# Kernel tuning notes

Hardware: AMD Instinct MI355X
Metric: run time of the kernel (lower is better)

The kernel has to match this reference:

```python
import jax, jax.numpy as jnp
import numpy as np
import math

D_MODEL = 512
N_HEADS = 8
D_FF = 2048
FACTOR = 5


def _layernorm(x, g, b, eps=1e-5):
    mu = jnp.mean(x, axis=-1, keepdims=True)
    var = jnp.mean((x - mu) ** 2, axis=-1, keepdims=True)
    return (x - mu) / jnp.sqrt(var + eps) * g + b


def setup_inputs() -> dict:
    key = jax.random.key(0)
    ks = jax.random.split(key, 12)
    B, L, D, F = 4, 2048, D_MODEL, D_FF
    sample_k = FACTOR * int(math.ceil(math.log(L)))  # 40
    x = jax.random.normal(ks[0], (B, L, D), dtype=jnp.float32)
    index_sample = jax.random.randint(ks[1], (L, sample_k), 0, L)
    s = 0.02
    inp = {
        'x': x,
        'index_sample': index_sample,
        'Wq': jax.random.normal(ks[2], (D, D), jnp.float32) * s, 'bq': jnp.zeros((D,), jnp.float32),
        'Wk': jax.random.normal(ks[3], (D, D), jnp.float32) * s, 'bk': jnp.zeros((D,), jnp.float32),
        'Wv': jax.random.normal(ks[4], (D, D), jnp.float32) * s, 'bv': jnp.zeros((D,), jnp.float32),
        'Wo': jax.random.normal(ks[5], (D, D), jnp.float32) * s, 'bo': jnp.zeros((D,), jnp.float32),
        'W1': jax.random.normal(ks[6], (F, D), jnp.float32) * s, 'b1': jnp.zeros((F,), jnp.float32),
        'W2': jax.random.normal(ks[7], (D, F), jnp.float32) * s, 'b2': jnp.zeros((D,), jnp.float32),
        'g1': jnp.ones((D,), jnp.float32), 'be1': jnp.zeros((D,), jnp.float32),
        'g2': jnp.ones((D,), jnp.float32), 'be2': jnp.zeros((D,), jnp.float32),
    }
    return inp


def _encoder_layer(x, index_sample, Wq, bq, Wk, bk, Wv, bv, Wo, bo, W1, b1, W2, b2, g1, be1, g2, be2):
    B, L, D = x.shape
    H = N_HEADS
    dk = D // H
    n_top = FACTOR * int(math.ceil(math.log(L)))  # 40; sparse branch since L*L > 40*40

    def split_heads(t):  # (B,L,D) -> (B,H,L,dk)
        return t.reshape(B, L, H, dk).transpose(0, 2, 1, 3)

    q = split_heads(x @ Wq.T + bq)
    k = split_heads(x @ Wk.T + bk)
    v = split_heads(x @ Wv.T + bv)

    # --- ProbSparse sampling: K_sample[b,h,i,j] = k[b,h,index_sample[i,j]] ---
    k_sample = k[:, :, index_sample, :]                      # (B,H,L,sample_k,dk)
    scores_sample = jnp.einsum('bhid,bhijd->bhij', q, k_sample)
    M = jnp.max(scores_sample, axis=-1) - jnp.sum(scores_sample, axis=-1) / L  # (B,H,L)
    _, top_idx = jax.lax.top_k(M, n_top)                     # (B,H,n_top)

    q_red = jnp.take_along_axis(q, top_idx[..., None], axis=2)  # (B,H,n_top,dk)
    scores_red = jnp.einsum('bhnd,bhkd->bhnk', q_red, k)        # NOTE: unscaled, as in source sparse branch

    bi = jnp.arange(B)[:, None, None]
    hi = jnp.arange(H)[None, :, None]
    scores = jnp.zeros((B, H, L, L), x.dtype).at[bi, hi, top_idx].set(scores_red)

    attn = jax.nn.softmax(scores, axis=-1)  # all-zero rows -> uniform (mean of V)
    ctx = jnp.einsum('bhqk,bhkd->bhqd', attn, v).transpose(0, 2, 1, 3).reshape(B, L, D)
    attn_out = ctx @ Wo.T + bo

    h1 = _layernorm(x + attn_out, g1, be1)
    ff = jax.nn.gelu(h1 @ W1.T + b1, approximate=False) @ W2.T + b2
    return _layernorm(h1 + ff, g2, be2)


def reference(x, index_sample, Wq, bq, Wk, bk, Wv, bv, Wo, bo, W1, b1, W2, b2, g1, be1, g2, be2):
    return _encoder_layer(x, index_sample, Wq, bq, Wk, bk, Wv, bv, Wo, bo,
                          W1, b1, W2, b2, g1, be1, g2, be2)
```

## Files before the change

kernel.cpp:

```cpp
#include <hip/hip_runtime.h>
#include <math.h>

#define L_SEQ   2048
#define DMODEL  512
#define NHEADS  8
#define DK      64
#define DFF     2048
#define BATCH   4
#define NTOP    40
#define MROWS   (BATCH*L_SEQ)
#define NCH     8
#define CHSZ    256
#define QPAD    48

typedef _Float16 f16;
typedef __attribute__((ext_vector_type(8))) _Float16 f16x8;
typedef __attribute__((ext_vector_type(8))) short    s16x8;
typedef __attribute__((ext_vector_type(4))) float    f32x4;

__device__ __forceinline__ ushort f2h_bits(float x) {
    f16 h = (f16)x;
    return __builtin_bit_cast(ushort, h);
}
__device__ __forceinline__ float h2f(ushort u) {
    return (float)__builtin_bit_cast(f16, u);
}

#define GLL16(gp, lp) \
    __builtin_amdgcn_global_load_lds((const __attribute__((address_space(1))) void*)(gp), \
                                     (__attribute__((address_space(3))) void*)(lp), 16, 0, 0)

template<int SPLIT3, int ACT, int OUTMODE>
__global__ __launch_bounds__(256)
void gemm16(const ushort* __restrict__ Ah, const ushort* __restrict__ Al,
            const ushort* __restrict__ Wh, const ushort* __restrict__ Wl,
            const float* __restrict__ bias,
            float* __restrict__ Cf, ushort* __restrict__ C16,
            int M, int N, int K)
{
    __shared__ __align__(16) ushort sAh[128*32];
    __shared__ __align__(16) ushort sBh[128*32];
    __shared__ __align__(16) ushort sAl[SPLIT3 ? 128*32 : 8];
    __shared__ __align__(16) ushort sBl[SPLIT3 ? 128*32 : 8];

    const int tid  = threadIdx.x;
    const int m0   = blockIdx.y * 128, n0 = blockIdx.x * 128;
    const int wid  = tid >> 6, lane = tid & 63;
    const int wr   = (wid >> 1) * 64;
    const int wc   = (wid & 1) * 64;
    const int lr   = lane & 15;
    const int ko   = (lane >> 4) * 8;

    f32x4 acc[4][4];
#pragma unroll
    for (int i = 0; i < 4; ++i)
#pragma unroll
        for (int j = 0; j < 4; ++j) acc[i][j] = (f32x4){0.f, 0.f, 0.f, 0.f};

    const int sr = tid >> 2, sc = (tid & 3) * 8;
    const size_t gA = (size_t)(m0 + sr) * K + sc;
    const size_t gB = (size_t)(n0 + sr) * K + sc;
    const int l0 = tid * 8, l1 = tid * 8 + 2048;

    for (int k0 = 0; k0 < K; k0 += 32) {
        GLL16(Ah + gA + k0,                sAh + l0);
        GLL16(Ah + gA + (size_t)64*K + k0, sAh + l1);
        GLL16(Wh + gB + k0,                sBh + l0);
        GLL16(Wh + gB + (size_t)64*K + k0, sBh + l1);
        if (SPLIT3) {
            GLL16(Al + gA + k0,                sAl + l0);
            GLL16(Al + gA + (size_t)64*K + k0, sAl + l1);
            GLL16(Wl + gB + k0,                sBl + l0);
            GLL16(Wl + gB + (size_t)64*K + k0, sBl + l1);
        }
        __syncthreads();

        f16x8 ah[4], bh[4], al[4], bl[4];
#pragma unroll
        for (int i = 0; i < 4; ++i) {
            ah[i] = *(const f16x8*)&sAh[(wr + i*16 + lr) * 32 + ko];
            bh[i] = *(const f16x8*)&sBh[(wc + i*16 + lr) * 32 + ko];
            if (SPLIT3) {
                al[i] = *(const f16x8*)&sAl[(wr + i*16 + lr) * 32 + ko];
                bl[i] = *(const f16x8*)&sBl[(wc + i*16 + lr) * 32 + ko];
            }
        }
#pragma unroll
        for (int i = 0; i < 4; ++i)
#pragma unroll
            for (int j = 0; j < 4; ++j) {
                acc[i][j] = __builtin_amdgcn_mfma_f32_16x16x32_f16(ah[i], bh[j], acc[i][j], 0, 0, 0);
                if (SPLIT3) {
                    acc[i][j] = __builtin_amdgcn_mfma_f32_16x16x32_f16(ah[i], bl[j], acc[i][j], 0, 0, 0);
                    acc[i][j] = __builtin_amdgcn_mfma_f32_16x16x32_f16(al[i], bh[j], acc[i][j], 0, 0, 0);
                }
            }
        __syncthreads();
    }

    const int r0 = m0 + wr + (lane >> 4) * 4;
#pragma unroll
    for (int i = 0; i < 4; ++i)
#pragma unroll
        for (int j = 0; j < 4; ++j) {
            const int col = n0 + wc + j * 16 + lr;
            const float bb = bias[col];
#pragma unroll
            for (int qq = 0; qq < 4; ++qq) {
                const int row = r0 + i * 16 + qq;
                float vv = acc[i][j][qq] + bb;
                if (ACT == 1) vv = 0.5f * vv * (1.f + erff(vv * 0.70710678118654752f));
                if (OUTMODE == 0 || OUTMODE == 2) Cf[(size_t)row * N + col] = vv;
                if (OUTMODE == 1 || OUTMODE == 2) C16[(size_t)row * N + col] = f2h_bits(vv);
                if (OUTMODE == 3)
                    C16[((size_t)(row >> 11) * 512 + (col >> 6) * 64 + (col & 63)) * 2048 + (row & 2047)] = f2h_bits(vv);
            }
        }
}

__device__ __forceinline__ void split8(const float* __restrict__ s,
                                       ushort* __restrict__ hi, ushort* __restrict__ lo)
{
    s16x8 h8, l8;
#pragma unroll
    for (int j = 0; j < 8; ++j) {
        float x = s[j];
        f16 hh = (f16)x;
        float r = x - (float)hh;
        f16 ll = (f16)r;
        h8[j] = (short)__builtin_bit_cast(ushort, hh);
        l8[j] = (short)__builtin_bit_cast(ushort, ll);
    }
    *(s16x8*)hi = h8;
    *(s16x8*)lo = l8;
}
__device__ __forceinline__ void cvt8(const float* __restrict__ s, ushort* __restrict__ d)
{
    s16x8 h8;
#pragma unroll
    for (int j = 0; j < 8; ++j) h8[j] = (short)f2h_bits(s[j]);
    *(s16x8*)d = h8;
}

__global__ __launch_bounds__(256)
void split_x(const float* __restrict__ x, ushort* __restrict__ xh, ushort* __restrict__ xl)
{
    const int t = blockIdx.x * 256 + threadIdx.x;
    split8(x + (size_t)t * 8, xh + (size_t)t * 8, xl + (size_t)t * 8);
}

__global__ __launch_bounds__(256)
void conv_weights(const float* __restrict__ Wq, const float* __restrict__ Wk,
                  const float* __restrict__ Wv, const float* __restrict__ Wo,
                  const float* __restrict__ W1, const float* __restrict__ W2,
                  ushort* wqh, ushort* wql, ushort* wkh, ushort* wkl,
                  ushort* wvh, ushort* woh, ushort* w1h, ushort* w2h)
{
    const int t = blockIdx.x * 256 + threadIdx.x;
    const int e = t * 8;
    const int S = DMODEL * DMODEL;
    if      (e < S)           split8(Wq + e,           wqh + e,           wql + e);
    else if (e < 2*S)         split8(Wk + (e -   S),   wkh + (e -   S),   wkl + (e -   S));
    else if (e < 3*S)         cvt8  (Wv + (e - 2*S),   wvh + (e - 2*S));
    else if (e < 4*S)         cvt8  (Wo + (e - 3*S),   woh + (e - 3*S));
    else if (e < 4*S + DFF*DMODEL) cvt8(W1 + (e - 4*S), w1h + (e - 4*S));
    else                      cvt8  (W2 + (e - 4*S - DFF*DMODEL), w2h + (e - 4*S - DFF*DMODEL));
}

__global__ __launch_bounds__(256, 4)
void sample_scores(const float* __restrict__ q, const float* __restrict__ k,
                   const int* __restrict__ idxs, float* __restrict__ Mout)
{
    __shared__ float4 qs[4][128];

    const int bid = blockIdx.x;
    const int xcd = bid & 7;
    const int b   = xcd >> 1;
    const int chunk = (bid >> 3) * 2 + (xcd & 1);
    const int wid = threadIdx.x >> 6, lane = threadIdx.x & 63;
    const int i = chunk * 4 + wid;
    const int jsub = lane >> 3, c = lane & 7;

    {
        const float4* qrow = (const float4*)&q[((size_t)(b * L_SEQ + i)) * DMODEL];
        qs[wid][lane]      = qrow[lane];
        qs[wid][lane + 64] = qrow[lane + 64];
    }
    __syncthreads();

    const float4* kb = (const float4*)&k[(size_t)b * L_SEQ * DMODEL];

    float mx = -1e30f, sm = 0.f;
#pragma unroll
    for (int jb = 0; jb < 5; ++jb) {
        const int kidx = idxs[i * NTOP + jb * 8 + jsub];
        const float4* krow = kb + (size_t)kidx * (DMODEL / 4);
        float hacc[8];
#pragma unroll
        for (int u = 0; u < 8; ++u) hacc[u] = 0.f;
#pragma unroll
        for (int t = 0; t < 16; ++t) {
            const int p = t * 8 + c;
            const float4 kv = krow[p];
            const float4 qv = qs[wid][p];
            float d = 0.f;
            d = fmaf(qv.x, kv.x, d);
            d = fmaf(qv.y, kv.y, d);
            d = fmaf(qv.z, kv.z, d);
            d = fmaf(qv.w, kv.w, d);
            hacc[t >> 1] += d;
        }
#pragma unroll
        for (int s = 1; s < 8; s <<= 1)
#pragma unroll
            for (int u = 0; u < 8; ++u) hacc[u] += __shfl_xor(hacc[u], s);
        float sel = hacc[0];
#pragma unroll
        for (int u = 1; u < 8; ++u) sel = (c == u) ? hacc[u] : sel;
        mx = fmaxf(mx, sel);
        sm += sel;
    }
#pragma unroll
    for (int s = 8; s < 64; s <<= 1) {
        mx = fmaxf(mx, __shfl_xor(mx, s));
        sm += __shfl_xor(sm, s);
    }
    if (jsub == 0)
        Mout[((size_t)(b * NHEADS + c)) * L_SEQ + i] = mx - sm * (1.0f / (float)L_SEQ);
}

__global__ __launch_bounds__(256)
void topk40(const float* __restrict__ Mstat, int* __restrict__ top_idx)
{
    const int bh = blockIdx.x;
    __shared__ float vals[L_SEQ];
    __shared__ float wv[4];
    __shared__ int   wi[4];
    const int tid = threadIdx.x;
    const int lane = tid & 63, wid = tid >> 6;
    for (int t = tid; t < L_SEQ; t += 256) vals[t] = Mstat[(size_t)bh * L_SEQ + t];
    __syncthreads();

    for (int n = 0; n < NTOP; ++n) {
        float bv = -1e30f; int bi = L_SEQ;
#pragma unroll
        for (int r = 0; r < 8; ++r) {
            const int t = tid + r * 256;
            float vvv = vals[t];
            if (vvv > bv) { bv = vvv; bi = t; }
        }
#pragma unroll
        for (int s = 32; s > 0; s >>= 1) {
            float ov = __shfl_xor(bv, s); int oi = __shfl_xor(bi, s);
            if (ov > bv || (ov == bv && oi < bi)) { bv = ov; bi = oi; }
        }
        if (lane == 0) { wv[wid] = bv; wi[wid] = bi; }
        __syncthreads();
        if (tid == 0) {
            float fb = wv[0]; int fi = wi[0];
#pragma unroll
            for (int w = 1; w < 4; ++w)
                if (wv[w] > fb || (wv[w] == fb && wi[w] < fi)) { fb = wv[w]; fi = wi[w]; }
            top_idx[bh * NTOP + n] = fi;
            vals[fi] = -1e30f;
        }
        __syncthreads();
    }
}

__global__ __launch_bounds__(256)
void vmean_kernel(const ushort* __restrict__ vt, float* __restrict__ vmean)
{
    const int bh = blockIdx.x;
    const int wid = threadIdx.x >> 6, lane = threadIdx.x & 63;
#pragma unroll
    for (int dd = 0; dd < 16; ++dd) {
        const int d = wid * 16 + dd;
        const ushort* row = vt + ((size_t)bh * 64 + d) * 2048;
        float s = 0.f;
#pragma unroll
        for (int it = 0; it < 4; ++it) {
            s16x8 vv = *(const s16x8*)&row[it * 512 + lane * 8];
#pragma unroll
            for (int j = 0; j < 8; ++j) s += h2f((ushort)vv[j]);
        }
#pragma unroll
        for (int st = 1; st < 64; st <<= 1) s += __shfl_xor(s, st);
        if (lane == 0) vmean[bh * DK + d] = s * (1.0f / (float)L_SEQ);
    }
}

__global__ __launch_bounds__(256)
void fill_ctx(const float* __restrict__ vmean, ushort* __restrict__ ctx)
{
    const int t = blockIdx.x * 256 + threadIdx.x;
    const int e = t * 8;
    const int col = e & (DMODEL - 1);
    const int row = e >> 9;
    const int b = row >> 11;
    const int h = col >> 6, d = col & 63;
    const float* vm = &vmean[(b * 8 + h) * DK + d];
    s16x8 o;
#pragma unroll
    for (int j = 0; j < 8; ++j) o[j] = (short)f2h_bits(vm[j]);
    *(s16x8*)&ctx[e] = o;
}

__global__ __launch_bounds__(256, 1)
void attn_flash(const float* __restrict__ q, const ushort* __restrict__ k16,
                const ushort* __restrict__ vt16, const int* __restrict__ top_idx,
                float* __restrict__ part_o, float* __restrict__ part_ml)
{
    __shared__ __align__(16) ushort K_lds [CHSZ * 64];
    __shared__ __align__(16) ushort Vt_lds[64 * CHSZ];
    __shared__ __align__(16) ushort Q_lds [QPAD * 64];
    __shared__ __align__(16) ushort P_lds [QPAD * CHSZ];
    __shared__ float red_max[4][QPAD];
    __shared__ float red_sum[4][QPAD];

    const int bh = blockIdx.x >> 3, ch = blockIdx.x & 7;
    const int b = bh >> 3, h = bh & 7;
    const int tid = threadIdx.x;
    const int wid = tid >> 6, lane = tid & 63;
    const int lr = lane & 15, ks = lane >> 4;

    {
        const ushort* kbase = k16 + ((size_t)b * L_SEQ + ch * CHSZ) * DMODEL + h * DK;
#pragma unroll
        for (int it = 0; it < 8; ++it) {
            const int qi2 = wid * 8 + it;
            const int row = qi2 * 8 + (lane >> 3);
            const int g = (lane & 7) ^ (row & 7);
            GLL16(kbase + (size_t)row * DMODEL + g * 8, K_lds + qi2 * 512 + lane * 8);
        }
        const ushort* vtb = vt16 + ((size_t)bh * 64) * 2048 + ch * CHSZ;
#pragma unroll
        for (int it = 0; it < 8; ++it) {
            const int qi2 = wid * 8 + it;
            const int drow = qi2 * 2 + (lane >> 5);
            const int g = (lane & 31) ^ (drow & 7);
            GLL16(vtb + (size_t)drow * 2048 + g * 8, Vt_lds + qi2 * 512 + lane * 8);
        }
    }
    if (tid < QPAD * 4) {
        const int r = tid >> 2, part = tid & 3;
        s16x8 w0, w1;
        if (r < NTOP) {
            const int qi = top_idx[bh * NTOP + r];
            const float* qp = q + ((size_t)b * L_SEQ + qi) * DMODEL + h * DK + part * 16;
#pragma unroll
            for (int u = 0; u < 8; ++u) { w0[u] = (short)f2h_bits(qp[u]); w1[u] = (short)f2h_bits(qp[u + 8]); }
        } else {
#pragma unroll
            for (int u = 0; u < 8; ++u) { w0[u] = 0; w1[u] = 0; }
        }
        const int g0 = part * 2;
        *(s16x8*)((char*)Q_lds + r * 128 + (((g0    ) ^ (r & 7)) << 4)) = w0;
        *(s16x8*)((char*)Q_lds + r * 128 + (((g0 + 1) ^ (r & 7)) << 4)) = w1;
    }
    __syncthreads();

    f16x8 af[3][2], bf[4][2];
#pragma unroll
    for (int i = 0; i < 3; ++i)
#pragma unroll
        for (int kt = 0; kt < 2; ++kt) {
            const int row = i * 16 + lr;
            const int g = (kt * 4 + ks) ^ (row & 7);
            af[i][kt] = *(const f16x8*)((const char*)Q_lds + row * 128 + g * 16);
        }
#pragma unroll
    for (int j = 0; j < 4; ++j)
#pragma unroll
        for (int kt = 0; kt < 2; ++kt) {
            const int row = wid * 64 + j * 16 + lr;
            const int g = (kt * 4 + ks) ^ (row & 7);
            bf[j][kt] = *(const f16x8*)((const char*)K_lds + row * 128 + g * 16);
        }
    f32x4 acc[3][4];
#pragma unroll
    for (int i = 0; i < 3; ++i)
#pragma unroll
        for (int j = 0; j < 4; ++j) acc[i][j] = (f32x4){0.f, 0.f, 0.f, 0.f};
#pragma unroll
    for (int i = 0; i < 3; ++i)
#pragma unroll
        for (int j = 0; j < 4; ++j)
#pragma unroll
            for (int kt = 0; kt < 2; ++kt)
                acc[i][j] = __builtin_amdgcn_mfma_f32_16x16x32_f16(af[i][kt], bf[j][kt], acc[i][j], 0, 0, 0);

    float mrow[3][4];
#pragma unroll
    for (int i = 0; i < 3; ++i)
#pragma unroll
        for (int r = 0; r < 4; ++r) {
            float m = acc[i][0][r];
            m = fmaxf(m, acc[i][1][r]); m = fmaxf(m, acc[i][2][r]); m = fmaxf(m, acc[i][3][r]);
            mrow[i][r] = m;
        }
#pragma unroll
    for (int s = 1; s < 16; s <<= 1)
#pragma unroll
        for (int i = 0; i < 3; ++i)
#pragma unroll
            for (int r = 0; r < 4; ++r) mrow[i][r] = fmaxf(mrow[i][r], __shfl_xor(mrow[i][r], s));
    if (lr == 0)
#pragma unroll
        for (int i = 0; i < 3; ++i)
#pragma unroll
            for (int r = 0; r < 4; ++r) red_max[wid][i * 16 + ks * 4 + r] = mrow[i][r];
    __syncthreads();
    float mc[3][4];
#pragma unroll
    for (int i = 0; i < 3; ++i)
#pragma unroll
        for (int r = 0; r < 4; ++r) {
            const int row = i * 16 + ks * 4 + r;
            mc[i][r] = fmaxf(fmaxf(red_max[0][row], red_max[1][row]),
                             fmaxf(red_max[2][row], red_max[3][row]));
        }

    float srow[3][4];
#pragma unroll
    for (int i = 0; i < 3; ++i)
#pragma unroll
        for (int r = 0; r < 4; ++r) srow[i][r] = 0.f;
#pragma unroll
    for (int i = 0; i < 3; ++i)
#pragma unroll
        for (int j = 0; j < 4; ++j)
#pragma unroll
            for (int r = 0; r < 4; ++r) {
                const float p = expf(acc[i][j][r] - mc[i][r]);
                srow[i][r] += p;
                const int row = i * 16 + ks * 4 + r;
                const int cc = wid * 64 + j * 16 + lr;
                const int g = (cc >> 3) ^ (row & 7);
                *(ushort*)((char*)P_lds + row * 512 + g * 16 + (cc & 7) * 2) = f2h_bits(p);
            }
#pragma unroll
    for (int s = 1; s < 16; s <<= 1)
#pragma unroll
        for (int i = 0; i < 3; ++i)
#pragma unroll
            for (int r = 0; r < 4; ++r) srow[i][r] += __shfl_xor(srow[i][r], s);
    if (lr == 0)
#pragma unroll
        for (int i = 0; i < 3; ++i)
#pragma unroll
            for (int r = 0; r < 4; ++r) red_sum[wid][i * 16 + ks * 4 + r] = srow[i][r];
    __syncthreads();

    if (wid == 0 && lr == 0) {
#pragma unroll
        for (int i = 0; i < 3; ++i)
#pragma unroll
            for (int r = 0; r < 4; ++r) {
                const int row = i * 16 + ks * 4 + r;
                const float lc = red_sum[0][row] + red_sum[1][row] + red_sum[2][row] + red_sum[3][row];
                part_ml[(((size_t)bh * NCH + ch) * QPAD + row) * 2 + 0] = mc[i][r];
                part_ml[(((size_t)bh * NCH + ch) * QPAD + row) * 2 + 1] = lc;
            }
    }

    f32x4 acc2[3];
#pragma unroll
    for (int i = 0; i < 3; ++i) acc2[i] = (f32x4){0.f, 0.f, 0.f, 0.f};
#pragma unroll
    for (int kt = 0; kt < 8; ++kt) {
        f16x8 vb;
        {
            const int row = wid * 16 + lr;
            const int g = (kt * 4 + ks) ^ (row & 7);
            vb = *(const f16x8*)((const char*)Vt_lds + row * 512 + g * 16);
        }
#pragma unroll
        for (int i = 0; i < 3; ++i) {
            const int row = i * 16 + lr;
            const int g = (kt * 4 + ks) ^ (row & 7);
            const f16x8 pa = *(const f16x8*)((const char*)P_lds + row * 512 + g * 16);
            acc2[i] = __builtin_amdgcn_mfma_f32_16x16x32_f16(pa, vb, acc2[i], 0, 0, 0);
        }
    }
#pragma unroll
    for (int i = 0; i < 3; ++i)
#pragma unroll
        for (int r = 0; r < 4; ++r) {
            const int row = i * 16 + ks * 4 + r;
            const int d = wid * 16 + lr;
            part_o[((((size_t)bh * NCH + ch) * QPAD) + row) * 64 + d] = acc2[i][r];
        }
}

__global__ __launch_bounds__(256)
void attn_combine(const float* __restrict__ part_o, const float* __restrict__ part_ml,
                  const int* __restrict__ top_idx, ushort* __restrict__ ctx)
{
    const int bh = blockIdx.x;
    const int b = bh >> 3, h = bh & 7;
    const int d = threadIdx.x & 63, qg = threadIdx.x >> 6;
#pragma unroll
    for (int u = 0; u < 10; ++u) {
        const int qq = qg * 10 + u;
        float mv[NCH], lv[NCH];
        float m = -1e30f;
#pragma unroll
        for (int c = 0; c < NCH; ++c) {
            mv[c] = part_ml[(((size_t)bh * NCH + c) * QPAD + qq) * 2 + 0];
            lv[c] = part_ml[(((size_t)bh * NCH + c) * QPAD + qq) * 2 + 1];
            m = fmaxf(m, mv[c]);
        }
        float l = 0.f, o = 0.f;
#pragma unroll
        for (int c = 0; c < NCH; ++c) {
            const float e = expf(mv[c] - m);
            l += e * lv[c];
            o += e * part_o[((((size_t)bh * NCH + c) * QPAD) + qq) * 64 + d];
        }
        const int qi = top_idx[bh * NTOP + qq];
        ctx[((size_t)b * L_SEQ + qi) * DMODEL + h * DK + d] = f2h_bits(o / l);
    }
}

template<int W16>
__global__ __launch_bounds__(256)
void ln_residual(const float* __restrict__ a, const float* __restrict__ bsrc,
                 const float* __restrict__ g, const float* __restrict__ be,
                 float* __restrict__ out, ushort* __restrict__ out16)
{
    const int row = blockIdx.x; const int tid = threadIdx.x;
    const size_t base = (size_t)row * DMODEL;
    float x0 = a[base + tid]       + bsrc[base + tid];
    float x1 = a[base + 256 + tid] + bsrc[base + 256 + tid];

    __shared__ float red[256];
    red[tid] = x0 + x1; __syncthreads();
    for (int st = 128; st > 0; st >>= 1) { if (tid < st) red[tid] += red[tid + st]; __syncthreads(); }
    const float mu = red[0] * (1.0f / (float)DMODEL);
    __syncthreads();

    const float d0 = x0 - mu, d1 = x1 - mu;
    red[tid] = d0 * d0 + d1 * d1; __syncthreads();
    for (int st = 128; st > 0; st >>= 1) { if (tid < st) red[tid] += red[tid + st]; __syncthreads(); }
    const float var = red[0] * (1.0f / (float)DMODEL);
    const float rstd = 1.0f / sqrtf(var + 1e-5f);

    const float y0 = d0 * rstd * g[tid]       + be[tid];
    const float y1 = d1 * rstd * g[256 + tid] + be[256 + tid];
    out[base + tid]       = y0;
    out[base + 256 + tid] = y1;
    if (W16) {
        out16[base + tid]       = f2h_bits(y0);
        out16[base + 256 + tid] = f2h_bits(y1);
    }
}

extern "C" void kernel_launch(void* const* d_in, const int* in_sizes, int n_in,
                              void* d_out, int out_size, void* d_ws, size_t ws_size,
                              hipStream_t stream)
{
    const float* x    = (const float*)d_in[0];
    const int*   idxs = (const int*)  d_in[1];
    const float* Wq = (const float*)d_in[2];  const float* bq = (const float*)d_in[3];
    const float* Wk = (const float*)d_in[4];  const float* bk = (const float*)d_in[5];
    const float* Wv = (const float*)d_in[6];  const float* bv = (const float*)d_in[7];
    const float* Wo = (const float*)d_in[8];  const float* bo = (const float*)d_in[9];
    const float* W1 = (const float*)d_in[10]; const float* b1 = (const float*)d_in[11];
    const float* W2 = (const float*)d_in[12]; const float* b2 = (const float*)d_in[13];
    const float* g1 = (const float*)d_in[14]; const float* be1= (const float*)d_in[15];
    const float* g2 = (const float*)d_in[16]; const float* be2= (const float*)d_in[17];

    const size_t MD = (size_t)MROWS * DMODEL;
    char* W = (char*)d_ws;
    ushort* xh   = (ushort*)(W);
    ushort* xl   = (ushort*)(W + 2*MD);
    float*  q    = (float*) (W + 4*MD);
    float*  k    = (float*) (W + 8*MD);
    ushort* k16  = (ushort*)(W + 12*MD);
    ushort* vt16 = (ushort*)(W + 14*MD);
    ushort* ctx16= (ushort*)(W + 16*MD);
    float*  att  = (float*) (W);
    float*  h1   = (float*) (W + 4*MD);
    ushort* h116 = (ushort*)(W + 8*MD);
    ushort* mid16= (ushort*)(W + 10*MD);
    ushort* wqh  = (ushort*)(W + 18*MD);
    ushort* wql  = wqh + DMODEL*DMODEL;
    ushort* wkh  = wql + DMODEL*DMODEL;
    ushort* wkl  = wkh + DMODEL*DMODEL;
    ushort* wvh  = wkl + DMODEL*DMODEL;
    ushort* woh  = wvh + DMODEL*DMODEL;
    ushort* w1h  = woh + DMODEL*DMODEL;
    ushort* w2h  = w1h + DFF*DMODEL;
    float*  Mstat = (float*)(w2h + DMODEL*DFF);
    float*  vmean = Mstat + (size_t)BATCH * NHEADS * L_SEQ;
    int*    top_idx = (int*)(vmean + BATCH * NHEADS * DK);
    float*  part_o  = (float*)(top_idx + BATCH * NHEADS * NTOP);
    float*  part_ml = part_o + (size_t)BATCH * NHEADS * NCH * QPAD * 64;

    dim3 blk(256);

    split_x<<<dim3(MD / 2048), blk, 0, stream>>>(x, xh, xl);
    conv_weights<<<dim3(1536), blk, 0, stream>>>(Wq, Wk, Wv, Wo, W1, W2,
                                                 wqh, wql, wkh, wkl, wvh, woh, w1h, w2h);

    gemm16<1,0,0><<<dim3(DMODEL/128, MROWS/128), blk, 0, stream>>>(xh, xl, wqh, wql, bq, q,   nullptr, MROWS, DMODEL, DMODEL);
    gemm16<1,0,2><<<dim3(DMODEL/128, MROWS/128), blk, 0, stream>>>(xh, xl, wkh, wkl, bk, k,   k16,     MROWS, DMODEL, DMODEL);
    gemm16<0,0,3><<<dim3(DMODEL/128, MROWS/128), blk, 0, stream>>>(xh, nullptr, wvh, nullptr, bv, nullptr, vt16, MROWS, DMODEL, DMODEL);

    sample_scores<<<dim3(2048), blk, 0, stream>>>(q, k, idxs, Mstat);
    topk40<<<dim3(BATCH*NHEADS), blk, 0, stream>>>(Mstat, top_idx);
    vmean_kernel<<<dim3(BATCH*NHEADS), blk, 0, stream>>>(vt16, vmean);
    fill_ctx<<<dim3(MD/2048), blk, 0, stream>>>(vmean, ctx16);
    attn_flash<<<dim3(BATCH*NHEADS*NCH), blk, 0, stream>>>(q, k16, vt16, top_idx, part_o, part_ml);
    attn_combine<<<dim3(BATCH*NHEADS), blk, 0, stream>>>(part_o, part_ml, top_idx, ctx16);

    gemm16<0,0,0><<<dim3(DMODEL/128, MROWS/128), blk, 0, stream>>>(ctx16, nullptr, woh, nullptr, bo, att, nullptr, MROWS, DMODEL, DMODEL);
    ln_residual<1><<<dim3(MROWS), blk, 0, stream>>>(x, att, g1, be1, h1, h116);

    gemm16<0,1,1><<<dim3(DFF/128, MROWS/128), blk, 0, stream>>>(h116, nullptr, w1h, nullptr, b1, nullptr, mid16, MROWS, DFF, DMODEL);
    gemm16<0,0,0><<<dim3(DMODEL/128, MROWS/128), blk, 0, stream>>>(mid16, nullptr, w2h, nullptr, b2, att, nullptr, MROWS, DMODEL, DFF);
    ln_residual<0><<<dim3(MROWS), blk, 0, stream>>>(h1, att, g2, be2, (float*)d_out, nullptr);
}
```

Baseline: 334.5 us.

## Batch QKV GEMMs into one launch, split-K the N=512 GEMMs, merge prep kernels

Merges the three Q/K/V projection GEMMs into one grid-z launch and folds the x-split and weight-conversion kernels into a single prep launch. The Wo and W2 GEMMs (N=512, 256 blocks) become split-K over two halves, writing two fp32 partials that the LayerNorm kernels sum together with the bias. The aim is to double block count on these small-grid GEMMs for better CU fill on a 256-CU part and to cut launch overhead. The cost is extra fp32 partial traffic and a larger workspace layout.

New measurement: 286.2 us. -14.5%, faster.

```diff
diff --git a/kernel.cpp b/kernel.cpp
--- a/kernel.cpp
+++ b/kernel.cpp
@@ -30,18 +30,27 @@
     __builtin_amdgcn_global_load_lds((const __attribute__((address_space(1))) void*)(gp), \
                                      (__attribute__((address_space(3))) void*)(lp), 16, 0, 0)
 
-template<int SPLIT3, int ACT, int OUTMODE>
-__global__ __launch_bounds__(256)
-void gemm16(const ushort* __restrict__ Ah, const ushort* __restrict__ Al,
-            const ushort* __restrict__ Wh, const ushort* __restrict__ Wl,
-            const float* __restrict__ bias,
-            float* __restrict__ Cf, ushort* __restrict__ C16,
-            int M, int N, int K)
+__global__ __launch_bounds__(256)
+void gemm_qkv(const ushort* __restrict__ xh, const ushort* __restrict__ xl,
+              const ushort* __restrict__ wqh, const ushort* __restrict__ wql,
+              const ushort* __restrict__ wkh, const ushort* __restrict__ wkl,
+              const ushort* __restrict__ wvh,
+              const float* __restrict__ bq, const float* __restrict__ bk,
+              const float* __restrict__ bv,
+              float* __restrict__ qo, float* __restrict__ kf,
+              ushort* __restrict__ k16, ushort* __restrict__ vt16)
 {
     __shared__ __align__(16) ushort sAh[128*32];
     __shared__ __align__(16) ushort sBh[128*32];
-    __shared__ __align__(16) ushort sAl[SPLIT3 ? 128*32 : 8];
-    __shared__ __align__(16) ushort sBl[SPLIT3 ? 128*32 : 8];
+    __shared__ __align__(16) ushort sAl[128*32];
+    __shared__ __align__(16) ushort sBl[128*32];
+
+    const int z = blockIdx.z;
+    const bool s3 = (z < 2);
+    const ushort* Wh = (z == 0) ? wqh : (z == 1) ? wkh : wvh;
+    const ushort* Wl = (z == 0) ? wql : wkl;
+    const float*  bias = (z == 0) ? bq : (z == 1) ? bk : bv;
+    const int K = DMODEL, N = DMODEL;
 
     const int tid  = threadIdx.x;
     const int m0   = blockIdx.y * 128, n0 = blockIdx.x * 128;
@@ -63,13 +72,13 @@
     const int l0 = tid * 8, l1 = tid * 8 + 2048;
 
     for (int k0 = 0; k0 < K; k0 += 32) {
-        GLL16(Ah + gA + k0,                sAh + l0);
-        GLL16(Ah + gA + (size_t)64*K + k0, sAh + l1);
+        GLL16(xh + gA + k0,                sAh + l0);
+        GLL16(xh + gA + (size_t)64*K + k0, sAh + l1);
         GLL16(Wh + gB + k0,                sBh + l0);
         GLL16(Wh + gB + (size_t)64*K + k0, sBh + l1);
-        if (SPLIT3) {
-            GLL16(Al + gA + k0,                sAl + l0);
-            GLL16(Al + gA + (size_t)64*K + k0, sAl + l1);
+        if (s3) {
+            GLL16(xl + gA + k0,                sAl + l0);
+            GLL16(xl + gA + (size_t)64*K + k0, sAl + l1);
             GLL16(Wl + gB + k0,                sBl + l0);
             GLL16(Wl + gB + (size_t)64*K + k0, sBl + l1);
         }
@@ -80,7 +89,7 @@
         for (int i = 0; i < 4; ++i) {
             ah[i] = *(const f16x8*)&sAh[(wr + i*16 + lr) * 32 + ko];
             bh[i] = *(const f16x8*)&sBh[(wc + i*16 + lr) * 32 + ko];
-            if (SPLIT3) {
+            if (s3) {
                 al[i] = *(const f16x8*)&sAl[(wr + i*16 + lr) * 32 + ko];
                 bl[i] = *(const f16x8*)&sBl[(wc + i*16 + lr) * 32 + ko];
             }
@@ -90,7 +99,7 @@
 #pragma unroll
             for (int j = 0; j < 4; ++j) {
                 acc[i][j] = __builtin_amdgcn_mfma_f32_16x16x32_f16(ah[i], bh[j], acc[i][j], 0, 0, 0);
-                if (SPLIT3) {
+                if (s3) {
                     acc[i][j] = __builtin_amdgcn_mfma_f32_16x16x32_f16(ah[i], bl[j], acc[i][j], 0, 0, 0);
                     acc[i][j] = __builtin_amdgcn_mfma_f32_16x16x32_f16(al[i], bh[j], acc[i][j], 0, 0, 0);
                 }
@@ -108,12 +117,147 @@
 #pragma unroll
             for (int qq = 0; qq < 4; ++qq) {
                 const int row = r0 + i * 16 + qq;
+                const float vv = acc[i][j][qq] + bb;
+                if (z == 0) {
+                    qo[(size_t)row * N + col] = vv;
+                } else if (z == 1) {
+                    kf [(size_t)row * N + col] = vv;
+                    k16[(size_t)row * N + col] = f2h_bits(vv);
+                } else {
+                    vt16[((size_t)(row >> 11) * 512 + (col >> 6) * 64 + (col & 63)) * 2048 + (row & 2047)] = f2h_bits(vv);
+                }
+            }
+        }
+}
+
+template<int ACT>
+__global__ __launch_bounds__(256)
+void gemm16(const ushort* __restrict__ Ah, const ushort* __restrict__ Wh,
+            const float* __restrict__ bias, ushort* __restrict__ C16,
+            int M, int N, int K)
+{
+    __shared__ __align__(16) ushort sAh[128*32];
+    __shared__ __align__(16) ushort sBh[128*32];
+
+    const int tid  = threadIdx.x;
+    const int m0   = blockIdx.y * 128, n0 = blockIdx.x * 128;
+    const int wid  = tid >> 6, lane = tid & 63;
+    const int wr   = (wid >> 1) * 64;
+    const int wc   = (wid & 1) * 64;
+    const int lr   = lane & 15;
+    const int ko   = (lane >> 4) * 8;
+
+    f32x4 acc[4][4];
+#pragma unroll
+    for (int i = 0; i < 4; ++i)
+#pragma unroll
+        for (int j = 0; j < 4; ++j) acc[i][j] = (f32x4){0.f, 0.f, 0.f, 0.f};
+
+    const int sr = tid >> 2, sc = (tid & 3) * 8;
+    const size_t gA = (size_t)(m0 + sr) * K + sc;
+    const size_t gB = (size_t)(n0 + sr) * K + sc;
+    const int l0 = tid * 8, l1 = tid * 8 + 2048;
+
+    for (int k0 = 0; k0 < K; k0 += 32) {
+        GLL16(Ah + gA + k0,                sAh + l0);
+        GLL16(Ah + gA + (size_t)64*K + k0, sAh + l1);
+        GLL16(Wh + gB + k0,                sBh + l0);
+        GLL16(Wh + gB + (size_t)64*K + k0, sBh + l1);
+        __syncthreads();
+
+        f16x8 ah[4], bh[4];
+#pragma unroll
+        for (int i = 0; i < 4; ++i) {
+            ah[i] = *(const f16x8*)&sAh[(wr + i*16 + lr) * 32 + ko];
+            bh[i] = *(const f16x8*)&sBh[(wc + i*16 + lr) * 32 + ko];
+        }
+#pragma unroll
+        for (int i = 0; i < 4; ++i)
+#pragma unroll
+            for (int j = 0; j < 4; ++j)
+                acc[i][j] = __builtin_amdgcn_mfma_f32_16x16x32_f16(ah[i], bh[j], acc[i][j], 0, 0, 0);
+        __syncthreads();
+    }
+
+    const int r0 = m0 + wr + (lane >> 4) * 4;
+#pragma unroll
+    for (int i = 0; i < 4; ++i)
+#pragma unroll
+        for (int j = 0; j < 4; ++j) {
+            const int col = n0 + wc + j * 16 + lr;
+            const float bb = bias[col];
+#pragma unroll
+            for (int qq = 0; qq < 4; ++qq) {
+                const int row = r0 + i * 16 + qq;
                 float vv = acc[i][j][qq] + bb;
                 if (ACT == 1) vv = 0.5f * vv * (1.f + erff(vv * 0.70710678118654752f));
-                if (OUTMODE == 0 || OUTMODE == 2) Cf[(size_t)row * N + col] = vv;
-                if (OUTMODE == 1 || OUTMODE == 2) C16[(size_t)row * N + col] = f2h_bits(vv);
-                if (OUTMODE == 3)
-                    C16[((size_t)(row >> 11) * 512 + (col >> 6) * 64 + (col & 63)) * 2048 + (row & 2047)] = f2h_bits(vv);
+                C16[(size_t)row * N + col] = f2h_bits(vv);
+            }
+        }
+}
+
+__global__ __launch_bounds__(256)
+void gemm_sk(const ushort* __restrict__ Ah, const ushort* __restrict__ Wh,
+             float* __restrict__ P0, float* __restrict__ P1, int K)
+{
+    __shared__ __align__(16) ushort sAh[128*32];
+    __shared__ __align__(16) ushort sBh[128*32];
+
+    const int z = blockIdx.z;
+    const int khalf = K >> 1, kbase = z * khalf;
+    const int N = DMODEL;
+    float* __restrict__ P = z ? P1 : P0;
+
+    const int tid  = threadIdx.x;
+    const int m0   = blockIdx.y * 128, n0 = blockIdx.x * 128;
+    const int wid  = tid >> 6, lane = tid & 63;
+    const int wr   = (wid >> 1) * 64;
+    const int wc   = (wid & 1) * 64;
+    const int lr   = lane & 15;
+    const int ko   = (lane >> 4) * 8;
+
+    f32x4 acc[4][4];
+#pragma unroll
+    for (int i = 0; i < 4; ++i)
+#pragma unroll
+        for (int j = 0; j < 4; ++j) acc[i][j] = (f32x4){0.f, 0.f, 0.f, 0.f};
+
+    const int sr = tid >> 2, sc = (tid & 3) * 8;
+    const size_t gA = (size_t)(m0 + sr) * K + sc;
+    const size_t gB = (size_t)(n0 + sr) * K + sc;
+    const int l0 = tid * 8, l1 = tid * 8 + 2048;
+
+    for (int k0 = kbase; k0 < kbase + khalf; k0 += 32) {
+        GLL16(Ah + gA + k0,                sAh + l0);
+        GLL16(Ah + gA + (size_t)64*K + k0, sAh + l1);
+        GLL16(Wh + gB + k0,                sBh + l0);
+        GLL16(Wh + gB + (size_t)64*K + k0, sBh + l1);
+        __syncthreads();
+
+        f16x8 ah[4], bh[4];
+#pragma unroll
+        for (int i = 0; i < 4; ++i) {
+            ah[i] = *(const f16x8*)&sAh[(wr + i*16 + lr) * 32 + ko];
+            bh[i] = *(const f16x8*)&sBh[(wc + i*16 + lr) * 32 + ko];
+        }
+#pragma unroll
+        for (int i = 0; i < 4; ++i)
+#pragma unroll
+            for (int j = 0; j < 4; ++j)
+                acc[i][j] = __builtin_amdgcn_mfma_f32_16x16x32_f16(ah[i], bh[j], acc[i][j], 0, 0, 0);
+        __syncthreads();
+    }
+
+    const int r0 = m0 + wr + (lane >> 4) * 4;
+#pragma unroll
+    for (int i = 0; i < 4; ++i)
+#pragma unroll
+        for (int j = 0; j < 4; ++j) {
+            const int col = n0 + wc + j * 16 + lr;
+#pragma unroll
+            for (int qq = 0; qq < 4; ++qq) {
+                const int row = r0 + i * 16 + qq;
+                P[(size_t)row * N + col] = acc[i][j][qq];
             }
         }
 }
@@ -143,20 +287,21 @@
 }
 
 __global__ __launch_bounds__(256)
-void split_x(const float* __restrict__ x, ushort* __restrict__ xh, ushort* __restrict__ xl)
-{
-    const int t = blockIdx.x * 256 + threadIdx.x;
-    split8(x + (size_t)t * 8, xh + (size_t)t * 8, xl + (size_t)t * 8);
-}
-
-__global__ __launch_bounds__(256)
-void conv_weights(const float* __restrict__ Wq, const float* __restrict__ Wk,
-                  const float* __restrict__ Wv, const float* __restrict__ Wo,
-                  const float* __restrict__ W1, const float* __restrict__ W2,
-                  ushort* wqh, ushort* wql, ushort* wkh, ushort* wkl,
-                  ushort* wvh, ushort* woh, ushort* w1h, ushort* w2h)
-{
-    const int t = blockIdx.x * 256 + threadIdx.x;
+void prep(const float* __restrict__ x,
+          const float* __restrict__ Wq, const float* __restrict__ Wk,
+          const float* __restrict__ Wv, const float* __restrict__ Wo,
+          const float* __restrict__ W1, const float* __restrict__ W2,
+          ushort* xh, ushort* xl,
+          ushort* wqh, ushort* wql, ushort* wkh, ushort* wkl,
+          ushort* wvh, ushort* woh, ushort* w1h, ushort* w2h)
+{
+    const int bid = blockIdx.x;
+    if (bid < 2048) {
+        const int t = bid * 256 + threadIdx.x;
+        split8(x + (size_t)t * 8, xh + (size_t)t * 8, xl + (size_t)t * 8);
+        return;
+    }
+    const int t = (bid - 2048) * 256 + threadIdx.x;
     const int e = t * 8;
     const int S = DMODEL * DMODEL;
     if      (e < S)           split8(Wq + e,           wqh + e,           wql + e);
@@ -525,14 +670,15 @@
 
 template<int W16>
 __global__ __launch_bounds__(256)
-void ln_residual(const float* __restrict__ a, const float* __restrict__ bsrc,
-                 const float* __restrict__ g, const float* __restrict__ be,
-                 float* __restrict__ out, ushort* __restrict__ out16)
+void ln2(const float* __restrict__ a, const float* __restrict__ p0,
+         const float* __restrict__ p1, const float* __restrict__ bias,
+         const float* __restrict__ g, const float* __restrict__ be,
+         float* __restrict__ out, ushort* __restrict__ out16)
 {
     const int row = blockIdx.x; const int tid = threadIdx.x;
     const size_t base = (size_t)row * DMODEL;
-    float x0 = a[base + tid]       + bsrc[base + tid];
-    float x1 = a[base + 256 + tid] + bsrc[base + 256 + tid];
+    float x0 = a[base + tid]       + p0[base + tid]       + p1[base + tid]       + bias[tid];
+    float x1 = a[base + 256 + tid] + p0[base + 256 + tid] + p1[base + 256 + tid] + bias[256 + tid];
 
     __shared__ float red[256];
     red[tid] = x0 + x1; __syncthreads();
@@ -573,18 +719,21 @@
 
     const size_t MD = (size_t)MROWS * DMODEL;
     char* W = (char*)d_ws;
-    ushort* xh   = (ushort*)(W);
-    ushort* xl   = (ushort*)(W + 2*MD);
-    float*  q    = (float*) (W + 4*MD);
-    float*  k    = (float*) (W + 8*MD);
-    ushort* k16  = (ushort*)(W + 12*MD);
-    ushort* vt16 = (ushort*)(W + 14*MD);
-    ushort* ctx16= (ushort*)(W + 16*MD);
-    float*  att  = (float*) (W);
-    float*  h1   = (float*) (W + 4*MD);
-    ushort* h116 = (ushort*)(W + 8*MD);
-    ushort* mid16= (ushort*)(W + 10*MD);
-    ushort* wqh  = (ushort*)(W + 18*MD);
+    ushort* xh    = (ushort*)(W);
+    ushort* xl    = (ushort*)(W + 2*MD);
+    float*  q     = (float*) (W + 4*MD);
+    float*  k     = (float*) (W + 8*MD);
+    ushort* k16   = (ushort*)(W + 12*MD);
+    ushort* vt16  = (ushort*)(W + 14*MD);
+    ushort* ctx16 = (ushort*)(W + 16*MD);
+    float*  wo_p0 = (float*) (W);
+    float*  wo_p1 = (float*) (W + 4*MD);
+    float*  h1    = (float*) (W + 8*MD);
+    ushort* h116  = (ushort*)(W + 12*MD);
+    ushort* mid16 = (ushort*)(W);
+    float*  w2_p0 = (float*) (W + 12*MD);
+    float*  w2_p1 = (float*) (W + 16*MD);
+    ushort* wqh   = (ushort*)(W + 20*MD);
     ushort* wql  = wqh + DMODEL*DMODEL;
     ushort* wkh  = wql + DMODEL*DMODEL;
     ushort* wkl  = wkh + DMODEL*DMODEL;
@@ -600,13 +749,11 @@
 
     dim3 blk(256);
 
-    split_x<<<dim3(MD / 2048), blk, 0, stream>>>(x, xh, xl);
-    conv_weights<<<dim3(1536), blk, 0, stream>>>(Wq, Wk, Wv, Wo, W1, W2,
-                                                 wqh, wql, wkh, wkl, wvh, woh, w1h, w2h);
-
-    gemm16<1,0,0><<<dim3(DMODEL/128, MROWS/128), blk, 0, stream>>>(xh, xl, wqh, wql, bq, q,   nullptr, MROWS, DMODEL, DMODEL);
-    gemm16<1,0,2><<<dim3(DMODEL/128, MROWS/128), blk, 0, stream>>>(xh, xl, wkh, wkl, bk, k,   k16,     MROWS, DMODEL, DMODEL);
-    gemm16<0,0,3><<<dim3(DMODEL/128, MROWS/128), blk, 0, stream>>>(xh, nullptr, wvh, nullptr, bv, nullptr, vt16, MROWS, DMODEL, DMODEL);
+    prep<<<dim3(2048 + 1536), blk, 0, stream>>>(x, Wq, Wk, Wv, Wo, W1, W2,
+                                                xh, xl, wqh, wql, wkh, wkl, wvh, woh, w1h, w2h);
+
+    gemm_qkv<<<dim3(DMODEL/128, MROWS/128, 3), blk, 0, stream>>>(
+        xh, xl, wqh, wql, wkh, wkl, wvh, bq, bk, bv, q, k, k16, vt16);
 
     sample_scores<<<dim3(2048), blk, 0, stream>>>(q, k, idxs, Mstat);
     topk40<<<dim3(BATCH*NHEADS), blk, 0, stream>>>(Mstat, top_idx);
@@ -615,10 +762,10 @@
     attn_flash<<<dim3(BATCH*NHEADS*NCH), blk, 0, stream>>>(q, k16, vt16, top_idx, part_o, part_ml);
     attn_combine<<<dim3(BATCH*NHEADS), blk, 0, stream>>>(part_o, part_ml, top_idx, ctx16);
 
-    gemm16<0,0,0><<<dim3(DMODEL/128, MROWS/128), blk, 0, stream>>>(ctx16, nullptr, woh, nullptr, bo, att, nullptr, MROWS, DMODEL, DMODEL);
-    ln_residual<1><<<dim3(MROWS), blk, 0, stream>>>(x, att, g1, be1, h1, h116);
-
-    gemm16<0,1,1><<<dim3(DFF/128, MROWS/128), blk, 0, stream>>>(h116, nullptr, w1h, nullptr, b1, nullptr, mid16, MROWS, DFF, DMODEL);
-    gemm16<0,0,0><<<dim3(DMODEL/128, MROWS/128), blk, 0, stream>>>(mid16, nullptr, w2h, nullptr, b2, att, nullptr, MROWS, DMODEL, DFF);
-    ln_residual<0><<<dim3(MROWS), blk, 0, stream>>>(h1, att, g2, be2, (float*)d_out, nullptr);
-}
+    gemm_sk<<<dim3(DMODEL/128, MROWS/128, 2), blk, 0, stream>>>(ctx16, woh, wo_p0, wo_p1, DMODEL);
+    ln2<1><<<dim3(MROWS), blk, 0, stream>>>(x, wo_p0, wo_p1, bo, g1, be1, h1, h116);
+
+    gemm16<1><<<dim3(DFF/128, MROWS/128), blk, 0, stream>>>(h116, w1h, b1, mid16, MROWS, DFF, DMODEL);
+    gemm_sk<<<dim3(DMODEL/128, MROWS/128, 2), blk, 0, stream>>>(mid16, w2h, w2_p0, w2_p1, DFF);
+    ln2<0><<<dim3(MROWS), blk, 0, stream>>>(h1, w2_p0, w2_p1, b2, g2, be2, (float*)d_out, nullptr);
+}
```
